# Performance work log

Hardware: AMD Instinct MI355X
Metric: run time of the kernel (lower is better)

The kernel has to match this reference:

```python
import jax, jax.numpy as jnp
import numpy as np

NE, NN, D, H, DH = 2048, 4096, 256, 8, 64
HD = H * DH
MAX_REL = 10


def setup_inputs() -> dict:
    key = jax.random.key(0)
    ks = jax.random.split(key, 10)
    inp = {}
    inp["hyperedge_features"] = jax.random.normal(ks[0], (NE, D), jnp.float32)
    inp["node_features"] = jax.random.normal(ks[1], (NN, D), jnp.float32)
    inp["incidence_matrix"] = jax.random.randint(ks[2], (NN, NE), 0, 2, jnp.int32)
    inp["node_types"] = jax.random.randint(ks[3], (NN,), 0, 2, jnp.int32)
    he_idx = jax.random.randint(ks[4], (NE,), 0, 4, jnp.int32)
    inp["hyperedge_types"] = jnp.array([0, 2, 3, 4], jnp.int32)[he_idx]  # valid query types
    s = 1.0 / np.sqrt(D)
    # per-type projection tables; query types indexed 0..4 (slot 1 unused, matches ModuleDict keys {0,2,3,4})
    inp["Wq"] = jax.random.normal(ks[5], (5, D, HD), jnp.float32) * s
    inp["Wk"] = jax.random.normal(ks[6], (2, D, HD), jnp.float32) * s
    inp["Wv"] = jax.random.normal(ks[7], (2, D, HD), jnp.float32) * s
    inp["Wo"] = jax.random.normal(ks[8], (HD + D, D), jnp.float32) * (1.0 / np.sqrt(HD + D))
    inp["bo"] = jnp.zeros((D,), jnp.float32)
    inp["gamma_e"] = jnp.ones((D,), jnp.float32)
    inp["beta_e"] = jnp.zeros((D,), jnp.float32)
    inp["gamma_n"] = jnp.ones((D,), jnp.float32)
    inp["beta_n"] = jnp.zeros((D,), jnp.float32)
    inp["rel_emb"] = jax.random.normal(ks[9], (2 * MAX_REL + 1, H), jnp.float32) * 0.02
    return inp


def _ln(x, g, b, eps=1e-5):
    m = jnp.mean(x, axis=-1, keepdims=True)
    v = jnp.var(x, axis=-1, keepdims=True)
    return (x - m) * jax.lax.rsqrt(v + eps) * g + b


def reference(hyperedge_features, node_features, incidence_matrix, node_types,
              hyperedge_types, Wq, Wk, Wv, Wo, bo, gamma_e, beta_e, gamma_n,
              beta_n, rel_emb):
    scale = DH ** 0.5
    e = _ln(hyperedge_features, gamma_e, beta_e)  # [NE, D]
    x = _ln(node_features, gamma_n, beta_n)       # [NN, D]
    # type-conditioned projections: project with every type table, gather per token
    q = jnp.einsum('nd,tdk->tnk', e, Wq)[hyperedge_types, jnp.arange(NE)]  # [NE, HD]
    k = jnp.einsum('nd,tdk->tnk', x, Wk)[node_types, jnp.arange(NN)]      # [NN, HD]
    v = jnp.einsum('nd,tdk->tnk', x, Wv)[node_types, jnp.arange(NN)]
    # 'n (h d) -> h n d'
    q = q.reshape(NE, H, DH).transpose(1, 0, 2)
    k = k.reshape(NN, H, DH).transpose(1, 0, 2)
    v = v.reshape(NN, H, DH).transpose(1, 0, 2)
    scores = jnp.einsum('hid,hjd->hij', q, k) / scale  # [H, NE, NN]
    mask = (incidence_matrix.T == 0)[None]             # [1, NE, NN]
    scores = jnp.where(mask, -jnp.inf, scores)
    rel = jnp.clip(jnp.arange(NE)[:, None] - jnp.arange(NN)[None, :], -MAX_REL, MAX_REL) + MAX_REL
    scores = scores + rel_emb[rel].transpose(2, 0, 1)  # pos bias added after mask, as in torch
    w = jax.nn.softmax(scores, axis=-1)                # dropout is identity in eval
    out = jnp.einsum('hij,hjd->hid', w, v)
    out = out.transpose(1, 0, 2).reshape(NE, HD)       # 'h n d -> n (h d)'
    out = jax.nn.silu(out)
    final = jnp.concatenate([e, out], axis=-1) @ Wo + bo
    return final, scores
```

## Files before the change

### kernel.cpp

```cpp
#include <hip/hip_runtime.h>
#include <cmath>

#define NE 2048
#define NN 4096
#define D 256
#define H 8
#define DH 64
#define HD 512
#define MAXREL 10
#define NREL 21
#define NEG_BIG -3.0e38f
#define L2E 1.44269504f

typedef __attribute__((ext_vector_type(8))) short bf16x8;
typedef __attribute__((ext_vector_type(4))) float f32x4;

__device__ inline short f2bf(float x) {
  union { float f; unsigned u; } c; c.f = x;
  unsigned r = (c.u + 0x7FFFu + ((c.u >> 16) & 1u)) >> 16;
  return (short)r;
}
__device__ inline short f2bf_t(float x) {
  return (short)(__float_as_uint(x) >> 16);
}
__device__ inline float bf2f(short s) {
  return __uint_as_float(((unsigned)(unsigned short)s) << 16);
}

__device__ inline void gl_lds16(const void* g, void* l) {
  __builtin_amdgcn_global_load_lds(
      (const __attribute__((address_space(1))) void*)g,
      (__attribute__((address_space(3))) void*)l, 16, 0, 0);
}

__global__ __launch_bounds__(256) void prep_all(
    const float* __restrict__ he, const int* __restrict__ htyp,
    const float* __restrict__ ge, const float* __restrict__ be,
    const float* __restrict__ nf, const int* __restrict__ ntyp,
    const float* __restrict__ gn, const float* __restrict__ bn,
    const int* __restrict__ inc, const float* __restrict__ Wq,
    const float* __restrict__ Wk, const float* __restrict__ Wv,
    const float* __restrict__ Wo,
    short* __restrict__ E2, short* __restrict__ X2,
    unsigned short* __restrict__ maskb, short* __restrict__ Wqf,
    short* __restrict__ Wkf, short* __restrict__ Wvf,
    short* __restrict__ Rf, short* __restrict__ Wof) {
  const int bid = blockIdx.x;
  const int t = threadIdx.x;
  __shared__ float part[4];
  __shared__ float bc[2];
  __shared__ float lnv[D];

  if (bid < NE) {
    const int i = bid;
    const float x = he[(size_t)i * D + t];
    float s = x;
#pragma unroll
    for (int off = 32; off > 0; off >>= 1) s += __shfl_down(s, off);
    if ((t & 63) == 0) part[t >> 6] = s;
    __syncthreads();
    if (t == 0) bc[0] = (part[0] + part[1] + part[2] + part[3]) * (1.0f / D);
    __syncthreads();
    const float mean = bc[0];
    const float dev = x - mean;
    float sq = dev * dev;
#pragma unroll
    for (int off = 32; off > 0; off >>= 1) sq += __shfl_down(sq, off);
    __syncthreads();
    if ((t & 63) == 0) part[t >> 6] = sq;
    __syncthreads();
    if (t == 0) bc[1] = (part[0] + part[1] + part[2] + part[3]) * (1.0f / D);
    __syncthreads();
    const float inv = rsqrtf(bc[1] + 1e-5f);
    const float v = dev * inv * ge[t] + be[t];
    lnv[t] = v;
    __syncthreads();
    const int ht = htyp[i];
    const int slot = (ht == 0) ? 0 : ht - 1;
    const int iin = i & 15, rt = i >> 4;
    {
      const int dd0 = 4 * t;
      const int kt = dd0 >> 5;
      const int lane = ((dd0 >> 2) & 3) * 16 + iin;
      const int e0 = ((dd0 >> 4) & 1) * 4;
      short v4[4];
#pragma unroll
      for (int u = 0; u < 4; ++u)
        v4[u] = ((dd0 >> 8) == slot) ? f2bf(lnv[(dd0 + u) & 255]) : (short)0;
      short* dst = E2 + ((size_t)(rt * 32 + kt) * 64 + lane) * 8 + e0;
      *(short4*)dst = make_short4(v4[0], v4[1], v4[2], v4[3]);
    }
    if (t < 128) {
      const int c0 = 2 * t;
      const int kt = c0 >> 5, kk = c0 & 31;
      const int l = ((kk >> 2) & 3) * 16 + iin;
      const int ee = (kk >> 4) * 4 + (kk & 3);
      short* dst = Rf + ((size_t)(rt * 24 + kt) * 64 + l) * 8 + ee;
      *(short2*)dst = make_short2(f2bf(lnv[c0]), f2bf(lnv[c0 + 1]));
    }
  } else if (bid < NE + NN) {
    const int j = bid - NE;
    const float x = nf[(size_t)j * D + t];
    float s = x;
#pragma unroll
    for (int off = 32; off > 0; off >>= 1) s += __shfl_down(s, off);
    if ((t & 63) == 0) part[t >> 6] = s;
    __syncthreads();
    if (t == 0) bc[0] = (part[0] + part[1] + part[2] + part[3]) * (1.0f / D);
    __syncthreads();
    const float mean = bc[0];
    const float dev = x - mean;
    float sq = dev * dev;
#pragma unroll
    for (int off = 32; off > 0; off >>= 1) sq += __shfl_down(sq, off);
    __syncthreads();
    if ((t & 63) == 0) part[t >> 6] = sq;
    __syncthreads();
    if (t == 0) bc[1] = (part[0] + part[1] + part[2] + part[3]) * (1.0f / D);
    __syncthreads();
    const float inv = rsqrtf(bc[1] + 1e-5f);
    lnv[t] = dev * inv * gn[t] + bn[t];
    __syncthreads();
    const int nt = ntyp[j];
    const int jin = j & 15, rt = j >> 4;
    const int dd0 = 2 * t;
    const int kt = dd0 >> 5;
    const int lane = ((dd0 >> 2) & 3) * 16 + jin;
    const int e0 = ((dd0 >> 4) & 1) * 4 + (dd0 & 3);
    const short v0 = ((dd0 >> 8) == nt) ? f2bf(lnv[dd0 & 255]) : (short)0;
    const short v1 = ((dd0 >> 8) == nt) ? f2bf(lnv[(dd0 + 1) & 255]) : (short)0;
    short* dst = X2 + ((size_t)(rt * 16 + kt) * 64 + lane) * 8 + e0;
    *(short2*)dst = make_short2(v0, v1);
  } else if (bid < NE + NN + NN / 2) {
    const int bb = bid - (NE + NN);
    const int it = t & 127;
    const int gj = bb * 2 + (t >> 7);
    const int* p = inc + (size_t)gj * NE + it * 16;
    unsigned m = 0;
#pragma unroll
    for (int r = 0; r < 16; ++r) m |= (p[r] != 0 ? 1u : 0u) << r;
    maskb[(size_t)it * NN + gj] = (unsigned short)m;
  } else if (bid < NE + NN + NN / 2 + 256) {
    const int bb = bid - (NE + NN + NN / 2);
    const int f = bb * 4 + (t >> 6);
    const int lane = t & 63;
    const int ct = f >> 5, kt = f & 31;
    const int c = ct * 16 + (lane & 15);
    const int khi = (lane >> 4) * 4;
    bf16x8 r;
#pragma unroll
    for (int e = 0; e < 8; ++e) {
      const int kk = (e >> 2) * 16 + khi + (e & 3);
      const int dd = kt * 32 + kk;
      const int sslot = dd >> 8;
      const int tt = (sslot == 0) ? 0 : sslot + 1;
      r[e] = f2bf(Wq[((size_t)tt * 256 + (dd & 255)) * 512 + c]);
    }
    *(bf16x8*)(Wqf + ((size_t)f * 64 + lane) * 8) = r;
  } else if (bid < NE + NN + NN / 2 + 256 + 128) {
    const int bb = bid - (NE + NN + NN / 2 + 256);
    const int f = bb * 4 + (t >> 6);
    const int lane = t & 63;
    const int ct = f >> 4, kt = f & 15;
    const int c = ct * 16 + (lane & 15);
    const int khi = (lane >> 4) * 4;
    bf16x8 rk, rv;
#pragma unroll
    for (int e = 0; e < 8; ++e) {
      const int kk = (e >> 2) * 16 + khi + (e & 3);
      const int dd = kt * 32 + kk;
      rk[e] = f2bf(Wk[(size_t)dd * 512 + c]);
      rv[e] = f2bf(Wv[(size_t)dd * 512 + c]);
    }
    *(bf16x8*)(Wkf + ((size_t)f * 64 + lane) * 8) = rk;
    *(bf16x8*)(Wvf + ((size_t)f * 64 + lane) * 8) = rv;
  } else {
    const int bb = bid - (NE + NN + NN / 2 + 256 + 128);
    const int f = bb * 4 + (t >> 6);
    const int lane = t & 63;
    const int ct = f / 24, kt = f - ct * 24;
    const int c = ct * 16 + (lane & 15);
    const int khi = (lane >> 4) * 4;
    bf16x8 r;
#pragma unroll
    for (int e = 0; e < 8; ++e) {
      const int kk = (e >> 2) * 16 + khi + (e & 3);
      const int dd = kt * 32 + kk;
      r[e] = f2bf(Wo[(size_t)dd * 256 + c]);
    }
    *(bf16x8*)(Wof + ((size_t)f * 64 + lane) * 8) = r;
  }
}

__global__ __launch_bounds__(256) void proj_all(
    const short* __restrict__ E2, const short* __restrict__ Wqf,
    short* __restrict__ Qp, const short* __restrict__ X2,
    const short* __restrict__ Wkf, const short* __restrict__ Wvf,
    short* __restrict__ Kp, short* __restrict__ Vp) {
  const int tid = threadIdx.x;
  const int w = tid >> 6, lane = tid & 63;
  __shared__ __align__(16) short tiles[2][12 * 512];

  if (blockIdx.x < 512) {
    const int RT0 = (blockIdx.x & 63) * 2;
    const int CT0 = (blockIdx.x >> 6) * 4;

#define QSTAGE(buf, ks)                                                        \
  do {                                                                         \
    const int rtl_ = w >> 1, ktl_ = w & 1;                                     \
    gl_lds16(E2 + ((size_t)((RT0 + rtl_) * 32 + (ks) * 2 + ktl_) * 64 + lane) * 8, \
             &tiles[buf][w * 512 + lane * 8]);                                 \
    gl_lds16(Wqf + ((size_t)((CT0 + (w >> 1)) * 32 + (ks) * 2 + (w & 1)) * 64 + lane) * 8, \
             &tiles[buf][(4 + w) * 512 + lane * 8]);                           \
    gl_lds16(Wqf + ((size_t)((CT0 + 2 + (w >> 1)) * 32 + (ks) * 2 + (w & 1)) * 64 + lane) * 8, \
             &tiles[buf][(8 + w) * 512 + lane * 8]);                           \
  } while (0)

    const int itl = w >> 1, ctp = w & 1;
    f32x4 acc[2] = {{0.f, 0.f, 0.f, 0.f}, {0.f, 0.f, 0.f, 0.f}};

    QSTAGE(0, 0);
    for (int ks = 0; ks < 16; ++ks) {
      const int cb = ks & 1;
      if (ks + 1 < 16) {
        QSTAGE(cb ^ 1, ks + 1);
        asm volatile("s_waitcnt vmcnt(3)" ::: "memory");
      } else {
        asm volatile("s_waitcnt vmcnt(0)" ::: "memory");
      }
      __builtin_amdgcn_s_barrier();
#pragma unroll
      for (int ktl = 0; ktl < 2; ++ktl) {
        const bf16x8 ef = *(const bf16x8*)&tiles[cb][(itl * 2 + ktl) * 512 + lane * 8];
#pragma unroll
        for (int ci = 0; ci < 2; ++ci) {
          const int ctl = ctp * 2 + ci;
          const bf16x8 qw = *(const bf16x8*)&tiles[cb][(4 + ctl * 2 + ktl) * 512 + lane * 8];
          acc[ci] = __builtin_amdgcn_mfma_f32_16x16x32_bf16(qw, ef, acc[ci], 0, 0, 0);
        }
      }
      __builtin_amdgcn_s_barrier();
    }

    const int it_g = RT0 + itl;
    const int ct_even = CT0 + ctp * 2;
    const int hh = ct_even >> 2, kc = (ct_even >> 1) & 1;
    bf16x8 fr;
#pragma unroll
    for (int r = 0; r < 4; ++r) { fr[r] = f2bf(acc[0][r]); fr[4 + r] = f2bf(acc[1][r]); }
    *(bf16x8*)(Qp + (((size_t)hh * (NE / 16) + it_g) * 2 + kc) * 512 + (size_t)lane * 8) = fr;
  } else {
    const int bb = blockIdx.x - 512;
    const int RT0 = (bb & 63) * 4;
    const int CT0 = (bb >> 6) * 4;

#define KVSTAGE(buf, kt)                                                       \
  do {                                                                         \
    gl_lds16(X2 + ((size_t)((RT0 + w) * 16 + (kt)) * 64 + lane) * 8,           \
             &tiles[buf][w * 512 + lane * 8]);                                 \
    gl_lds16(Wkf + ((size_t)((CT0 + w) * 16 + (kt)) * 64 + lane) * 8,          \
             &tiles[buf][(4 + w) * 512 + lane * 8]);                           \
    gl_lds16(Wvf + ((size_t)((CT0 + w) * 16 + (kt)) * 64 + lane) * 8,          \
             &tiles[buf][(8 + w) * 512 + lane * 8]);                           \
  } while (0)

    const int wr = w >> 1, wc = w & 1;
    f32x4 accK[2][2], accV[2][2];
#pragma unroll
    for (int a = 0; a < 2; ++a)
#pragma unroll
      for (int b = 0; b < 2; ++b) {
        accK[a][b] = (f32x4){0.f, 0.f, 0.f, 0.f};
        accV[a][b] = (f32x4){0.f, 0.f, 0.f, 0.f};
      }

    KVSTAGE(0, 0);
    for (int kt = 0; kt < 16; ++kt) {
      const int cb = kt & 1;
      if (kt + 1 < 16) {
        KVSTAGE(cb ^ 1, kt + 1);
        asm volatile("s_waitcnt vmcnt(3)" ::: "memory");
      } else {
        asm volatile("s_waitcnt vmcnt(0)" ::: "memory");
      }
      __builtin_amdgcn_s_barrier();
      bf16x8 xf[2], kf[2], vf[2];
#pragma unroll
      for (int p = 0; p < 2; ++p) {
        xf[p] = *(const bf16x8*)&tiles[cb][(wr * 2 + p) * 512 + lane * 8];
        kf[p] = *(const bf16x8*)&tiles[cb][(4 + wc * 2 + p) * 512 + lane * 8];
        vf[p] = *(const bf16x8*)&tiles[cb][(8 + wc * 2 + p) * 512 + lane * 8];
      }
#pragma unroll
      for (int ci = 0; ci < 2; ++ci)
#pragma unroll
        for (int ji = 0; ji < 2; ++ji) {
          accK[ci][ji] = __builtin_amdgcn_mfma_f32_16x16x32_bf16(kf[ci], xf[ji], accK[ci][ji], 0, 0, 0);
          accV[ji][ci] = __builtin_amdgcn_mfma_f32_16x16x32_bf16(xf[ji], vf[ci], accV[ji][ci], 0, 0, 0);
        }
      __builtin_amdgcn_s_barrier();
    }

    const int ct_even = CT0 + wc * 2;
    const int hh = ct_even >> 2, kc = (ct_even >> 1) & 1;
#pragma unroll
    for (int ji = 0; ji < 2; ++ji) {
      const int jt16 = RT0 + wr * 2 + ji;
      bf16x8 fr;
#pragma unroll
      for (int r = 0; r < 4; ++r) { fr[r] = f2bf(accK[0][ji][r]); fr[4 + r] = f2bf(accK[1][ji][r]); }
      *(bf16x8*)(Kp + (((((size_t)hh * 64 + (jt16 >> 2)) * 4 + (jt16 & 3)) * 2 + kc) * 512) + (size_t)lane * 8) = fr;
    }
    const int jt_even = RT0 + wr * 2;
    const int jt64 = jt_even >> 2, kcv = (jt_even >> 1) & 1;
#pragma unroll
    for (int ci = 0; ci < 2; ++ci) {
      const int ctg = CT0 + wc * 2 + ci;
      const int hhv = ctg >> 2, dh16 = ctg & 3;
      bf16x8 fr;
#pragma unroll
      for (int r = 0; r < 4; ++r) { fr[r] = f2bf(accV[0][ci][r]); fr[4 + r] = f2bf(accV[1][ci][r]); }
      *(bf16x8*)(Vp + ((((size_t)hhv * 64 + jt64) * 4 + dh16) * 2 + kcv) * 512 + (size_t)lane * 8) = fr;
    }
  }
}

__global__ __launch_bounds__(256) void attn_mfma(
    const short* __restrict__ Qp, const short* __restrict__ Kp,
    const short* __restrict__ Vp, const unsigned short* __restrict__ maskb,
    const float* __restrict__ rel_emb, float* __restrict__ scores,
    short* __restrict__ po, float* __restrict__ pm, float* __restrict__ pl,
    int tps) {
  const int h = blockIdx.y;
  const int split = blockIdx.z;
  const int tid = threadIdx.x;
  const int wid = tid >> 6;
  const int lane = tid & 63;
  const int i0w = blockIdx.x * 64 + wid * 16;
  const int gi = i0w + (lane & 15);
  const int gi15 = lane & 15;
  const int lhi4 = (lane >> 4) * 4;
  const int jt0 = split * tps;
  const int itw = i0w >> 4;

  __shared__ __align__(16) short Kt[2][4096];
  __shared__ __align__(16) short Vt[2][4096];
  __shared__ __align__(16) unsigned short Ms[4][2][64];
  __shared__ float relb[NREL];

  if (tid < NREL) relb[tid] = rel_emb[tid * H + h];
  __syncthreads();

  const size_t qbase = (((size_t)h * (NE / 16) + itw) * 2) * 512 + (size_t)lane * 8;
  const bf16x8 qf0 = *(const bf16x8*)(Qp + qbase);
  const bf16x8 qf1 = *(const bf16x8*)(Qp + qbase + 512);

  const short* kgh = Kp + (size_t)h * 64 * 4096;
  const short* vgh = Vp + (size_t)h * 64 * 4096;
  const unsigned short* mgh = maskb + (size_t)itw * NN;

#define STAGE(buf, jt)                                              \
  do {                                                              \
    const short* kg_ = kgh + (size_t)(jt) * 4096 + tid * 8;         \
    const short* vg_ = vgh + (size_t)(jt) * 4096 + tid * 8;         \
    gl_lds16(kg_, &Kt[buf][tid * 8]);                               \
    gl_lds16(kg_ + 2048, &Kt[buf][2048 + tid * 8]);                 \
    gl_lds16(vg_, &Vt[buf][tid * 8]);                               \
    gl_lds16(vg_ + 2048, &Vt[buf][2048 + tid * 8]);                 \
    if (lane < 8)                                                   \
      gl_lds16(mgh + (size_t)(jt) * 64 + lane * 8,                  \
               &Ms[wid][buf][lane * 8]);                            \
  } while (0)

  STAGE(0, jt0);
  asm volatile("s_waitcnt vmcnt(0)" ::: "memory");
  __builtin_amdgcn_s_barrier();

  float m_run = -INFINITY, l_run = 0.f;
  f32x4 o0 = {0.f, 0.f, 0.f, 0.f}, o1 = o0, o2 = o0, o3 = o0;

  for (int t = 0; t < tps; ++t) {
    const int jb = jt0 + t;
    const int b = t & 1;
    if (t + 1 < tps) {
      STAGE(b ^ 1, jb + 1);
      if (t > 0) { asm volatile("s_waitcnt vmcnt(9)" ::: "memory"); }
    } else {
      if (t > 0) { asm volatile("s_waitcnt vmcnt(4)" ::: "memory"); }
    }
    __builtin_amdgcn_s_barrier();

    const int j0 = jb * 64;
    const float bc0 = relb[0], bc20 = relb[20];
    const bool allhi = (j0 > i0w + 15 + MAXREL);
    const bool alllo = (j0 + 63 < i0w - MAXREL);

    float lg[4][4];
#pragma unroll
    for (int ms = 0; ms < 4; ++ms) {
      const bf16x8 ka = *(const bf16x8*)&Kt[b][(ms * 2 + 0) * 512 + lane * 8];
      const bf16x8 kb = *(const bf16x8*)&Kt[b][(ms * 2 + 1) * 512 + lane * 8];
      f32x4 sf = {0.f, 0.f, 0.f, 0.f};
      __builtin_amdgcn_s_setprio(1);
      sf = __builtin_amdgcn_mfma_f32_16x16x32_bf16(ka, qf0, sf, 0, 0, 0);
      sf = __builtin_amdgcn_mfma_f32_16x16x32_bf16(kb, qf1, sf, 0, 0, 0);
      __builtin_amdgcn_s_setprio(0);
      const int jb0 = j0 + ms * 16 + lhi4;
      const uint2 mw = *(const uint2*)&Ms[wid][b][ms * 16 + lhi4];
#pragma unroll
      for (int r = 0; r < 4; ++r) {
        const int gj = jb0 + r;
        float bias;
        if (allhi) bias = bc0;
        else if (alllo) bias = bc20;
        else {
          int dd = gi - gj;
          dd = dd < -MAXREL ? -MAXREL : (dd > MAXREL ? MAXREL : dd);
          bias = relb[dd + MAXREL];
        }
        const unsigned word = (r < 2) ? mw.x : mw.y;
        const unsigned ok = (word >> ((r & 1) * 16 + gi15)) & 1u;
        lg[ms][r] = ok ? fmaf(sf[r], 0.125f, bias) : -INFINITY;
      }
      f32x4 sv;
      sv[0] = fmaxf(lg[ms][0], NEG_BIG);
      sv[1] = fmaxf(lg[ms][1], NEG_BIG);
      sv[2] = fmaxf(lg[ms][2], NEG_BIG);
      sv[3] = fmaxf(lg[ms][3], NEG_BIG);
      *(f32x4*)(scores + ((size_t)h * NE + gi) * NN + jb0) = sv;
    }

    float tmax = -INFINITY;
#pragma unroll
    for (int ms = 0; ms < 4; ++ms)
#pragma unroll
      for (int r = 0; r < 4; ++r) tmax = fmaxf(tmax, lg[ms][r]);
    tmax = fmaxf(tmax, __shfl_xor(tmax, 16));
    tmax = fmaxf(tmax, __shfl_xor(tmax, 32));
    const float mnew = fmaxf(m_run, tmax);
    const float rs = (m_run == mnew) ? 1.f : exp2f((m_run - mnew) * L2E);
    float p[4][4];
    float ps = 0.f;
#pragma unroll
    for (int ms = 0; ms < 4; ++ms)
#pragma unroll
      for (int r = 0; r < 4; ++r) {
        const float v = lg[ms][r];
        const float pe = (v == -INFINITY) ? 0.f : exp2f((v - mnew) * L2E);
        p[ms][r] = pe;
        ps += pe;
      }
    l_run = l_run * rs + ps;
    m_run = mnew;
    if (!__all(rs == 1.0f)) { o0 *= rs; o1 *= rs; o2 *= rs; o3 *= rs; }

    bf16x8 pb0, pb1;
    pb0[0] = f2bf_t(p[0][0]); pb0[1] = f2bf_t(p[0][1]); pb0[2] = f2bf_t(p[0][2]); pb0[3] = f2bf_t(p[0][3]);
    pb0[4] = f2bf_t(p[1][0]); pb0[5] = f2bf_t(p[1][1]); pb0[6] = f2bf_t(p[1][2]); pb0[7] = f2bf_t(p[1][3]);
    pb1[0] = f2bf_t(p[2][0]); pb1[1] = f2bf_t(p[2][1]); pb1[2] = f2bf_t(p[2][2]); pb1[3] = f2bf_t(p[2][3]);
    pb1[4] = f2bf_t(p[3][0]); pb1[5] = f2bf_t(p[3][1]); pb1[6] = f2bf_t(p[3][2]); pb1[7] = f2bf_t(p[3][3]);

    __builtin_amdgcn_s_setprio(1);
    o0 = __builtin_amdgcn_mfma_f32_16x16x32_bf16(*(const bf16x8*)&Vt[b][0 * 512 + lane * 8], pb0, o0, 0, 0, 0);
    o0 = __builtin_amdgcn_mfma_f32_16x16x32_bf16(*(const bf16x8*)&Vt[b][1 * 512 + lane * 8], pb1, o0, 0, 0, 0);
    o1 = __builtin_amdgcn_mfma_f32_16x16x32_bf16(*(const bf16x8*)&Vt[b][2 * 512 + lane * 8], pb0, o1, 0, 0, 0);
    o1 = __builtin_amdgcn_mfma_f32_16x16x32_bf16(*(const bf16x8*)&Vt[b][3 * 512 + lane * 8], pb1, o1, 0, 0, 0);
    o2 = __builtin_amdgcn_mfma_f32_16x16x32_bf16(*(const bf16x8*)&Vt[b][4 * 512 + lane * 8], pb0, o2, 0, 0, 0);
    o2 = __builtin_amdgcn_mfma_f32_16x16x32_bf16(*(const bf16x8*)&Vt[b][5 * 512 + lane * 8], pb1, o2, 0, 0, 0);
    o3 = __builtin_amdgcn_mfma_f32_16x16x32_bf16(*(const bf16x8*)&Vt[b][6 * 512 + lane * 8], pb0, o3, 0, 0, 0);
    o3 = __builtin_amdgcn_mfma_f32_16x16x32_bf16(*(const bf16x8*)&Vt[b][7 * 512 + lane * 8], pb1, o3, 0, 0, 0);
    __builtin_amdgcn_s_setprio(0);

    asm volatile("s_waitcnt lgkmcnt(0)" ::: "memory");
    __builtin_amdgcn_s_barrier();
  }

  l_run += __shfl_xor(l_run, 16);
  l_run += __shfl_xor(l_run, 32);
  const size_t pbase = ((size_t)split * H + h) * NE + gi;
  if (lane < 16) { pm[pbase] = m_run; pl[pbase] = l_run; }
  short* pob = po + pbase * DH + lhi4;
  *(short4*)(pob +  0) = make_short4(f2bf(o0[0]), f2bf(o0[1]), f2bf(o0[2]), f2bf(o0[3]));
  *(short4*)(pob + 16) = make_short4(f2bf(o1[0]), f2bf(o1[1]), f2bf(o1[2]), f2bf(o1[3]));
  *(short4*)(pob + 32) = make_short4(f2bf(o2[0]), f2bf(o2[1]), f2bf(o2[2]), f2bf(o2[3]));
  *(short4*)(pob + 48) = make_short4(f2bf(o3[0]), f2bf(o3[1]), f2bf(o3[2]), f2bf(o3[3]));
}

__global__ __launch_bounds__(256) void combine_kernel(
    const short* __restrict__ po, const float* __restrict__ pm,
    const float* __restrict__ pl, short* __restrict__ Rf, int splits) {
  const int g = blockIdx.x * 8 + (threadIdx.x >> 5);
  const int dh0 = (threadIdx.x & 31) * 2;
  const int h = g >> 11;
  const int i = g & (NE - 1);
  float M = -INFINITY;
  for (int s = 0; s < splits; ++s)
    M = fmaxf(M, pm[((size_t)s * H + h) * NE + i]);
  float L = 0.f, o0 = 0.f, o1 = 0.f;
  for (int s = 0; s < splits; ++s) {
    const size_t pb = ((size_t)s * H + h) * NE + i;
    const float ms = pm[pb];
    if (ms > -INFINITY) {
      const float wgt = exp2f((ms - M) * L2E);
      L += wgt * pl[pb];
      const short2 ov = *(const short2*)&po[pb * DH + dh0];
      o0 += wgt * bf2f(ov.x);
      o1 += wgt * bf2f(ov.y);
    }
  }
  const float a0 = o0 / L, a1 = o1 / L;
  const float s0 = a0 / (1.f + expf(-a0));
  const float s1 = a1 / (1.f + expf(-a1));
  const int col = 256 + h * DH + dh0;
  const int kt = col >> 5, kk = col & 31;
  const int l = ((kk >> 2) & 3) * 16 + (i & 15);
  const int ee = (kk >> 4) * 4 + (kk & 3);
  short* dst = Rf + ((size_t)((i >> 4) * 24 + kt) * 64 + l) * 8 + ee;
  *(short2*)dst = make_short2(f2bf(s0), f2bf(s1));
}

__global__ __launch_bounds__(256) void final_mfma(
    const short* __restrict__ Rf, const short* __restrict__ Wof,
    const float* __restrict__ bo, float* __restrict__ out) {
  const int tid = threadIdx.x;
  const int w = tid >> 6, lane = tid & 63;
  const int RT0 = blockIdx.x * 2;
  const int CT0 = blockIdx.y * 4;
  __shared__ __align__(16) short tiles[2][12 * 512];

#define FSTAGE(buf, ks)                                                        \
  do {                                                                         \
    const int rtl_ = w >> 1, ktl_ = w & 1;                                     \
    gl_lds16(Rf + ((size_t)((RT0 + rtl_) * 24 + (ks) * 2 + ktl_) * 64 + lane) * 8, \
             &tiles[buf][w * 512 + lane * 8]);                                 \
    gl_lds16(Wof + ((size_t)((CT0 + (w >> 1)) * 24 + (ks) * 2 + (w & 1)) * 64 + lane) * 8, \
             &tiles[buf][(4 + w) * 512 + lane * 8]);                           \
    gl_lds16(Wof + ((size_t)((CT0 + 2 + (w >> 1)) * 24 + (ks) * 2 + (w & 1)) * 64 + lane) * 8, \
             &tiles[buf][(8 + w) * 512 + lane * 8]);                           \
  } while (0)

  const int itl = w >> 1, ctp = w & 1;
  f32x4 acc[2] = {{0.f, 0.f, 0.f, 0.f}, {0.f, 0.f, 0.f, 0.f}};

  FSTAGE(0, 0);
  for (int ks = 0; ks < 12; ++ks) {
    const int cb = ks & 1;
    if (ks + 1 < 12) {
      FSTAGE(cb ^ 1, ks + 1);
      asm volatile("s_waitcnt vmcnt(3)" ::: "memory");
    } else {
      asm volatile("s_waitcnt vmcnt(0)" ::: "memory");
    }
    __builtin_amdgcn_s_barrier();
#pragma unroll
    for (int ktl = 0; ktl < 2; ++ktl) {
      const bf16x8 rf = *(const bf16x8*)&tiles[cb][(itl * 2 + ktl) * 512 + lane * 8];
#pragma unroll
      for (int ci = 0; ci < 2; ++ci) {
        const int ctl = ctp * 2 + ci;
        const bf16x8 wf = *(const bf16x8*)&tiles[cb][(4 + ctl * 2 + ktl) * 512 + lane * 8];
        acc[ci] = __builtin_amdgcn_mfma_f32_16x16x32_bf16(wf, rf, acc[ci], 0, 0, 0);
      }
    }
    __builtin_amdgcn_s_barrier();
  }

  const int gi = (RT0 + itl) * 16 + (lane & 15);
  const int lhi4 = (lane >> 4) * 4;
#pragma unroll
  for (int ci = 0; ci < 2; ++ci) {
    const int c0 = (CT0 + ctp * 2 + ci) * 16 + lhi4;
    float4 o;
    o.x = acc[ci][0] + bo[c0];
    o.y = acc[ci][1] + bo[c0 + 1];
    o.z = acc[ci][2] + bo[c0 + 2];
    o.w = acc[ci][3] + bo[c0 + 3];
    *(float4*)(out + (size_t)gi * D + c0) = o;
  }
}

extern "C" void kernel_launch(void* const* d_in, const int* in_sizes, int n_in,
                              void* d_out, int out_size, void* d_ws, size_t ws_size,
                              hipStream_t stream) {
  (void)in_sizes; (void)n_in; (void)out_size;
  const float* he   = (const float*)d_in[0];
  const float* nf   = (const float*)d_in[1];
  const int*   inc  = (const int*)d_in[2];
  const int*   ntyp = (const int*)d_in[3];
  const int*   htyp = (const int*)d_in[4];
  const float* Wq   = (const float*)d_in[5];
  const float* Wk   = (const float*)d_in[6];
  const float* Wv   = (const float*)d_in[7];
  const float* Wo   = (const float*)d_in[8];
  const float* bo   = (const float*)d_in[9];
  const float* ge   = (const float*)d_in[10];
  const float* be   = (const float*)d_in[11];
  const float* gn   = (const float*)d_in[12];
  const float* bn   = (const float*)d_in[13];
  const float* rel  = (const float*)d_in[14];

  float* outf = (float*)d_out;
  float* outs = outf + (size_t)NE * D;

  short* X2   = (short*)d_ws;
  short* E2   = X2 + (size_t)NN * 512;
  short* Wkf  = E2 + (size_t)NE * 1024;
  short* Wvf  = Wkf + (size_t)512 * 512;
  short* Wqf  = Wvf + (size_t)512 * 512;
  short* Qp   = Wqf + (size_t)512 * 1024;
  short* Kp   = Qp + (size_t)NE * HD;
  short* Vp   = Kp + (size_t)NN * HD;
  short* Rf   = Vp + (size_t)NN * HD;
  short* Wof  = Rf + (size_t)128 * 24 * 512;
  unsigned short* maskb = (unsigned short*)(Wof + (size_t)384 * 512);
  short* po   = (short*)(maskb + (size_t)(NE / 16) * NN);

  const size_t used_bytes = (size_t)((char*)po - (char*)d_ws);
  int splits = 8;
  while (splits > 1 &&
         used_bytes + (size_t)splits * H * NE * (DH * 2 + 8) > ws_size)
    splits >>= 1;
  float* pm = (float*)(po + (size_t)splits * H * NE * DH);
  float* pl = pm + (size_t)splits * H * NE;
  const int tps = NN / 64 / splits;

  prep_all<<<NE + NN + NN / 2 + 256 + 128 + 96, 256, 0, stream>>>(
      he, htyp, ge, be, nf, ntyp, gn, bn, inc, Wq, Wk, Wv, Wo,
      E2, X2, maskb, Wqf, Wkf, Wvf, Rf, Wof);
  proj_all<<<1024, 256, 0, stream>>>(E2, Wqf, Qp, X2, Wkf, Wvf, Kp, Vp);
  attn_mfma<<<dim3(NE / 64, H, splits), 256, 0, stream>>>(
      Qp, Kp, Vp, maskb, rel, outs, po, pm, pl, tps);
  combine_kernel<<<NE * H / 8, 256, 0, stream>>>(po, pm, pl, Rf, splits);
  final_mfma<<<dim3(64, 4), 256, 0, stream>>>(Rf, Wof, bo, outf);
}
```

Before: 150.8 us.

## Load K/V tiles directly from global memory instead of LDS double buffering

Removes the shared-memory double-buffered staging of K, V and mask tiles, along with the barriers, waitcnts and setprio hints. Each wave now loads its K/V MFMA fragments and mask words straight from global memory (through cache) inside the loop. This frees LDS and removes block-level synchronisation, which may raise occupancy. In exchange, the four waves of a block each fetch the same K/V data redundantly, and global load latency is no longer hidden by explicit prefetch.

```diff
diff --git a/kernel.cpp b/kernel.cpp
--- a/kernel.cpp
+++ b/kernel.cpp
@@ -334,20 +334,15 @@
   const int h = blockIdx.y;
   const int split = blockIdx.z;
   const int tid = threadIdx.x;
-  const int wid = tid >> 6;
   const int lane = tid & 63;
-  const int i0w = blockIdx.x * 64 + wid * 16;
+  const int i0w = blockIdx.x * 64 + (tid >> 6) * 16;
   const int gi = i0w + (lane & 15);
   const int gi15 = lane & 15;
   const int lhi4 = (lane >> 4) * 4;
   const int jt0 = split * tps;
   const int itw = i0w >> 4;
 
-  __shared__ __align__(16) short Kt[2][4096];
-  __shared__ __align__(16) short Vt[2][4096];
-  __shared__ __align__(16) unsigned short Ms[4][2][64];
   __shared__ float relb[NREL];
-
   if (tid < NREL) relb[tid] = rel_emb[tid * H + h];
   __syncthreads();
 
@@ -355,58 +350,35 @@
   const bf16x8 qf0 = *(const bf16x8*)(Qp + qbase);
   const bf16x8 qf1 = *(const bf16x8*)(Qp + qbase + 512);
 
-  const short* kgh = Kp + (size_t)h * 64 * 4096;
-  const short* vgh = Vp + (size_t)h * 64 * 4096;
+  const short* kgh = Kp + (size_t)h * 64 * 4096 + lane * 8;
+  const short* vgh = Vp + (size_t)h * 64 * 4096 + lane * 8;
   const unsigned short* mgh = maskb + (size_t)itw * NN;
-
-#define STAGE(buf, jt)                                              \
-  do {                                                              \
-    const short* kg_ = kgh + (size_t)(jt) * 4096 + tid * 8;         \
-    const short* vg_ = vgh + (size_t)(jt) * 4096 + tid * 8;         \
-    gl_lds16(kg_, &Kt[buf][tid * 8]);                               \
-    gl_lds16(kg_ + 2048, &Kt[buf][2048 + tid * 8]);                 \
-    gl_lds16(vg_, &Vt[buf][tid * 8]);                               \
-    gl_lds16(vg_ + 2048, &Vt[buf][2048 + tid * 8]);                 \
-    if (lane < 8)                                                   \
-      gl_lds16(mgh + (size_t)(jt) * 64 + lane * 8,                  \
-               &Ms[wid][buf][lane * 8]);                            \
-  } while (0)
-
-  STAGE(0, jt0);
-  asm volatile("s_waitcnt vmcnt(0)" ::: "memory");
-  __builtin_amdgcn_s_barrier();
 
   float m_run = -INFINITY, l_run = 0.f;
   f32x4 o0 = {0.f, 0.f, 0.f, 0.f}, o1 = o0, o2 = o0, o3 = o0;
 
   for (int t = 0; t < tps; ++t) {
     const int jb = jt0 + t;
-    const int b = t & 1;
-    if (t + 1 < tps) {
-      STAGE(b ^ 1, jb + 1);
-      if (t > 0) { asm volatile("s_waitcnt vmcnt(9)" ::: "memory"); }
-    } else {
-      if (t > 0) { asm volatile("s_waitcnt vmcnt(4)" ::: "memory"); }
-    }
-    __builtin_amdgcn_s_barrier();
-
+    const size_t toff = (size_t)jb * 4096;
     const int j0 = jb * 64;
     const float bc0 = relb[0], bc20 = relb[20];
     const bool allhi = (j0 > i0w + 15 + MAXREL);
     const bool alllo = (j0 + 63 < i0w - MAXREL);
 
+    uint2 mw[4];
+#pragma unroll
+    for (int ms = 0; ms < 4; ++ms)
+      mw[ms] = *(const uint2*)(mgh + toff / 64 + ms * 16 + lhi4);
+
     float lg[4][4];
 #pragma unroll
     for (int ms = 0; ms < 4; ++ms) {
-      const bf16x8 ka = *(const bf16x8*)&Kt[b][(ms * 2 + 0) * 512 + lane * 8];
-      const bf16x8 kb = *(const bf16x8*)&Kt[b][(ms * 2 + 1) * 512 + lane * 8];
+      const bf16x8 ka = *(const bf16x8*)(kgh + toff + (ms * 2 + 0) * 512);
+      const bf16x8 kb = *(const bf16x8*)(kgh + toff + (ms * 2 + 1) * 512);
       f32x4 sf = {0.f, 0.f, 0.f, 0.f};
-      __builtin_amdgcn_s_setprio(1);
       sf = __builtin_amdgcn_mfma_f32_16x16x32_bf16(ka, qf0, sf, 0, 0, 0);
       sf = __builtin_amdgcn_mfma_f32_16x16x32_bf16(kb, qf1, sf, 0, 0, 0);
-      __builtin_amdgcn_s_setprio(0);
       const int jb0 = j0 + ms * 16 + lhi4;
-      const uint2 mw = *(const uint2*)&Ms[wid][b][ms * 16 + lhi4];
 #pragma unroll
       for (int r = 0; r < 4; ++r) {
         const int gj = jb0 + r;
@@ -418,7 +390,7 @@
           dd = dd < -MAXREL ? -MAXREL : (dd > MAXREL ? MAXREL : dd);
           bias = relb[dd + MAXREL];
         }
-        const unsigned word = (r < 2) ? mw.x : mw.y;
+        const unsigned word = (r < 2) ? mw[ms].x : mw[ms].y;
         const unsigned ok = (word >> ((r & 1) * 16 + gi15)) & 1u;
         lg[ms][r] = ok ? fmaf(sf[r], 0.125f, bias) : -INFINITY;
       }
@@ -460,19 +432,14 @@
     pb1[0] = f2bf_t(p[2][0]); pb1[1] = f2bf_t(p[2][1]); pb1[2] = f2bf_t(p[2][2]); pb1[3] = f2bf_t(p[2][3]);
     pb1[4] = f2bf_t(p[3][0]); pb1[5] = f2bf_t(p[3][1]); pb1[6] = f2bf_t(p[3][2]); pb1[7] = f2bf_t(p[3][3]);
 
-    __builtin_amdgcn_s_setprio(1);
-    o0 = __builtin_amdgcn_mfma_f32_16x16x32_bf16(*(const bf16x8*)&Vt[b][0 * 512 + lane * 8], pb0, o0, 0, 0, 0);
-    o0 = __builtin_amdgcn_mfma_f32_16x16x32_bf16(*(const bf16x8*)&Vt[b][1 * 512 + lane * 8], pb1, o0, 0, 0, 0);
-    o1 = __builtin_amdgcn_mfma_f32_16x16x32_bf16(*(const bf16x8*)&Vt[b][2 * 512 + lane * 8], pb0, o1, 0, 0, 0);
-    o1 = __builtin_amdgcn_mfma_f32_16x16x32_bf16(*(const bf16x8*)&Vt[b][3 * 512 + lane * 8], pb1, o1, 0, 0, 0);
-    o2 = __builtin_amdgcn_mfma_f32_16x16x32_bf16(*(const bf16x8*)&Vt[b][4 * 512 + lane * 8], pb0, o2, 0, 0, 0);
-    o2 = __builtin_amdgcn_mfma_f32_16x16x32_bf16(*(const bf16x8*)&Vt[b][5 * 512 + lane * 8], pb1, o2, 0, 0, 0);
-    o3 = __builtin_amdgcn_mfma_f32_16x16x32_bf16(*(const bf16x8*)&Vt[b][6 * 512 + lane * 8], pb0, o3, 0, 0, 0);
-    o3 = __builtin_amdgcn_mfma_f32_16x16x32_bf16(*(const bf16x8*)&Vt[b][7 * 512 + lane * 8], pb1, o3, 0, 0, 0);
-    __builtin_amdgcn_s_setprio(0);
-
-    asm volatile("s_waitcnt lgkmcnt(0)" ::: "memory");
-    __builtin_amdgcn_s_barrier();
+    o0 = __builtin_amdgcn_mfma_f32_16x16x32_bf16(*(const bf16x8*)(vgh + toff + 0 * 512), pb0, o0, 0, 0, 0);
+    o0 = __builtin_amdgcn_mfma_f32_16x16x32_bf16(*(const bf16x8*)(vgh + toff + 1 * 512), pb1, o0, 0, 0, 0);
+    o1 = __builtin_amdgcn_mfma_f32_16x16x32_bf16(*(const bf16x8*)(vgh + toff + 2 * 512), pb0, o1, 0, 0, 0);
+    o1 = __builtin_amdgcn_mfma_f32_16x16x32_bf16(*(const bf16x8*)(vgh + toff + 3 * 512), pb1, o1, 0, 0, 0);
+    o2 = __builtin_amdgcn_mfma_f32_16x16x32_bf16(*(const bf16x8*)(vgh + toff + 4 * 512), pb0, o2, 0, 0, 0);
+    o2 = __builtin_amdgcn_mfma_f32_16x16x32_bf16(*(const bf16x8*)(vgh + toff + 5 * 512), pb1, o2, 0, 0, 0);
+    o3 = __builtin_amdgcn_mfma_f32_16x16x32_bf16(*(const bf16x8*)(vgh + toff + 6 * 512), pb0, o3, 0, 0, 0);
+    o3 = __builtin_amdgcn_mfma_f32_16x16x32_bf16(*(const bf16x8*)(vgh + toff + 7 * 512), pb1, o3, 0, 0, 0);
   }
 
   l_run += __shfl_xor(l_run, 16);
```

Result: slower. 161.9 us (+7.4%).
